# Optimization experiments

Hardware: AMD Instinct MI355X
Metric: run time of the kernel (lower is better)

Reference implementation:

```python
import jax, jax.numpy as jnp
import numpy as np

N = 4096  # input_size == output_size
B = 8192  # batch rows


def setup_inputs() -> dict:
    key = jax.random.key(0)
    k1, k2, k3 = jax.random.split(key, 3)
    inp = jax.random.normal(k1, (B, N), dtype=jnp.float32)
    weight = jax.random.normal(k2, (N, N), dtype=jnp.float32)
    bias = jax.random.normal(k3, (N,), dtype=jnp.float32)
    return {"input": inp, "weight": weight, "bias": bias}


def reference(input, weight, bias):
    # torch: mm(input, weight * eye(N, N)) + bias
    # weight * eye zeroes everything except the diagonal, so the GEMM
    # reduces exactly to an elementwise scale by diag(weight) plus bias.
    diag_w = jnp.diagonal(weight)  # [N]
    return input * diag_w + bias
```

## Files before the change

### kernel.cpp

```cpp
#include <hip/hip_runtime.h>


#define NCOL 4096
#define NROW 8192

__global__ __launch_bounds__(256)
void extract_diag_kernel(const float* __restrict__ w, float* __restrict__ d) {
    int i = blockIdx.x * blockDim.x + threadIdx.x;
    if (i < NCOL) {
        d[i] = w[(size_t)i * NCOL + i];
    }
}

__global__ __launch_bounds__(256)
void scale_bias_kernel(const float4* __restrict__ in,
                       const float4* __restrict__ diag4,
                       const float4* __restrict__ bias4,
                       float4* __restrict__ out,
                       long total4) {
    const long stride = (long)gridDim.x * blockDim.x;
    for (long i = (long)blockIdx.x * blockDim.x + threadIdx.x; i < total4; i += stride) {
        const int j = (int)(i & (NCOL / 4 - 1));
        const float4 x = in[i];
        const float4 d = diag4[j];
        const float4 b = bias4[j];
        float4 o;
        o.x = fmaf(x.x, d.x, b.x);
        o.y = fmaf(x.y, d.y, b.y);
        o.z = fmaf(x.z, d.z, b.z);
        o.w = fmaf(x.w, d.w, b.w);
        out[i] = o;
    }
}

extern "C" void kernel_launch(void* const* d_in, const int* in_sizes, int n_in,
                              void* d_out, int out_size, void* d_ws, size_t ws_size,
                              hipStream_t stream) {
    const float* input  = (const float*)d_in[0];
    const float* weight = (const float*)d_in[1];
    const float* bias   = (const float*)d_in[2];
    float* out  = (float*)d_out;
    float* diag = (float*)d_ws;

    extract_diag_kernel<<<(NCOL + 255) / 256, 256, 0, stream>>>(weight, diag);

    const long total4 = (long)NROW * NCOL / 4;
    const int block = 256;
    const int grid = 2048;
    scale_bias_kernel<<<grid, block, 0, stream>>>(
        (const float4*)input, (const float4*)diag, (const float4*)bias,
        (float4*)out, total4);
}
```

Measured before the change: 50.70 us.

## Hoist diag/bias per thread, row-strided loop with nontemporal loads and stores

Restructures the scale-bias kernel so each thread owns a fixed column quad and walks 16 rows strided by 512 rows. The diagonal and bias values are loaded once into registers instead of every iteration. Input loads and output stores use nontemporal builtins to avoid polluting cache with the streamed 128MB+128MB traffic. The grid becomes 2048 blocks with a fully unrolled fixed trip count, which raises per-thread memory-level parallelism at the cost of more registers.

```diff
diff --git a/kernel.cpp b/kernel.cpp
--- a/kernel.cpp
+++ b/kernel.cpp
@@ -3,33 +3,43 @@
 
 #define NCOL 4096
 #define NROW 8192
+#define QCOL (NCOL / 4)
+#define ROWGROUPS 512
+#define ITERS (NROW / ROWGROUPS)
+
+typedef float f4 __attribute__((ext_vector_type(4)));
 
 __global__ __launch_bounds__(256)
 void extract_diag_kernel(const float* __restrict__ w, float* __restrict__ d) {
     int i = blockIdx.x * blockDim.x + threadIdx.x;
     if (i < NCOL) {
-        d[i] = w[(size_t)i * NCOL + i];
+        d[i] = w[(size_t)i * (NCOL + 1)];
     }
 }
 
 __global__ __launch_bounds__(256)
-void scale_bias_kernel(const float4* __restrict__ in,
-                       const float4* __restrict__ diag4,
-                       const float4* __restrict__ bias4,
-                       float4* __restrict__ out,
-                       long total4) {
-    const long stride = (long)gridDim.x * blockDim.x;
-    for (long i = (long)blockIdx.x * blockDim.x + threadIdx.x; i < total4; i += stride) {
-        const int j = (int)(i & (NCOL / 4 - 1));
-        const float4 x = in[i];
-        const float4 d = diag4[j];
-        const float4 b = bias4[j];
-        float4 o;
+void scale_bias_kernel(const f4* __restrict__ in,
+                       const f4* __restrict__ diag4,
+                       const f4* __restrict__ bias4,
+                       f4* __restrict__ out) {
+    const int t  = blockIdx.x * blockDim.x + threadIdx.x;
+    const int j  = t & (QCOL - 1);
+    const int r0 = t >> 10;
+
+    const f4 d = diag4[j];
+    const f4 b = bias4[j];
+
+    size_t idx = (size_t)r0 * QCOL + j;
+#pragma unroll
+    for (int k = 0; k < ITERS; ++k) {
+        f4 x = __builtin_nontemporal_load(&in[idx]);
+        f4 o;
         o.x = fmaf(x.x, d.x, b.x);
         o.y = fmaf(x.y, d.y, b.y);
         o.z = fmaf(x.z, d.z, b.z);
         o.w = fmaf(x.w, d.w, b.w);
-        out[i] = o;
+        __builtin_nontemporal_store(o, &out[idx]);
+        idx += (size_t)ROWGROUPS * QCOL;
     }
 }
 
@@ -44,10 +54,9 @@
 
     extract_diag_kernel<<<(NCOL + 255) / 256, 256, 0, stream>>>(weight, diag);
 
-    const long total4 = (long)NROW * NCOL / 4;
     const int block = 256;
-    const int grid = 2048;
+    const int grid  = (NROW / ITERS) * QCOL / block;
     scale_bias_kernel<<<grid, block, 0, stream>>>(
-        (const float4*)input, (const float4*)diag, (const float4*)bias,
-        (float4*)out, total4);
+        (const f4*)input, (const f4*)diag, (const f4*)bias,
+        (f4*)out);
 }
```

New measurement: 69.55 us. +37.2%, slower.
